# Optimization experiments

Hardware: AMD Instinct MI355X
Metric: run time of the kernel (lower is better)

## Reference

```python
import jax, jax.numpy as jnp
import numpy as np

N_NODES = 100000

def _sage_conv(h, src, dst, Wl, bl, Wr):
    # PyG SAGEConv (mean aggr): out = lin_l(mean_{j in N(i)} h_j) + lin_r(h_i)
    msg = h[src]                                            # [E, H] gather
    agg = jax.ops.segment_sum(msg, dst, num_segments=N_NODES)   # [N, H] scatter-add
    cnt = jax.ops.segment_sum(jnp.ones((src.shape[0],), h.dtype), dst, num_segments=N_NODES)
    mean = agg / jnp.maximum(cnt, 1.0)[:, None]
    return mean @ Wl + bl + h @ Wr

def setup_inputs() -> dict:
    key = jax.random.key(0)
    ks = jax.random.split(key, 12)
    IN, H, C, E = 256, 128, 40, 1600000
    s = 0.05
    return {
        "x": jax.random.normal(ks[0], (N_NODES, IN), jnp.float32),
        "edge_index": jax.random.randint(ks[1], (2, E), 0, N_NODES, jnp.int32),
        "W_pre": jax.random.normal(ks[2], (IN, H), jnp.float32) * s,
        "b_pre": jnp.zeros((H,), jnp.float32),
        "Wl0": jax.random.normal(ks[3], (H, H), jnp.float32) * s,
        "bl0": jnp.zeros((H,), jnp.float32),
        "Wr0": jax.random.normal(ks[4], (H, H), jnp.float32) * s,
        "Wl1": jax.random.normal(ks[5], (H, H), jnp.float32) * s,
        "bl1": jnp.zeros((H,), jnp.float32),
        "Wr1": jax.random.normal(ks[6], (H, H), jnp.float32) * s,
        "W_post": jax.random.normal(ks[7], (H, C), jnp.float32) * s,
        "b_post": jnp.zeros((C,), jnp.float32),
    }

def reference(x, edge_index, W_pre, b_pre, Wl0, bl0, Wr0, Wl1, bl1, Wr1, W_post, b_post):
    src, dst = edge_index[0], edge_index[1]
    h = x @ W_pre + b_pre                       # pre Linear
    # two SAGEConv layers + relu (dropout is identity in eval mode)
    h = jax.nn.relu(_sage_conv(h, src, dst, Wl0, bl0, Wr0))
    h = jax.nn.relu(_sage_conv(h, src, dst, Wl1, bl1, Wr1))
    logits = h @ W_post + b_post                # post Linear
    return jax.nn.log_softmax(logits, axis=1)
```

## Files before the change

### kernel.cpp

```cpp
#include <hip/hip_runtime.h>
#include <hip/hip_bf16.h>
#include <math.h>

#define N_NODES 100000
#define IN_F 256
#define HID 128
#define NCLS 40

#define NB 782
#define BN 128
#define NC 448
#define CSZ2 3584
#define CAP 4096

typedef __attribute__((ext_vector_type(8))) short short8;
typedef __attribute__((ext_vector_type(4))) float f32x4;

__device__ __forceinline__ short f2bf(float f){
  union { float f; unsigned u; } x; x.f = f;
  unsigned r = (x.u + 0x7fffu + ((x.u >> 16) & 1u)) >> 16;
  return (short)r;
}
__device__ __forceinline__ float bf2f(unsigned short u){
  union { unsigned u; float f; } x; x.u = ((unsigned)u) << 16;
  return x.f;
}

__global__ __launch_bounds__(256) void k_wprep(
    const float* __restrict__ Wpre, const float* __restrict__ Wl0,
    const float* __restrict__ Wr0,  const float* __restrict__ Wl1,
    const float* __restrict__ Wr1,  const float* __restrict__ Wpost,
    unsigned short* __restrict__ img)
{
  const int g = blockIdx.x*256 + threadIdx.x;
  if(g >= 13056) return;
  const int base = g*8;
  unsigned short v[8];
  if(base < 98304){
    const int which = base >> 15;
    const int idx = base & 32767;
    const int l = (idx >> 3) & 63, kb = (idx >> 9) & 7, ct = idx >> 12;
    const int col = ct*16 + (l & 15);
    const float* Wsrc; int kbase;
    if(which == 0){ Wsrc = Wpre; kbase = kb*32 + (l>>4)*8; }
    else{
      Wsrc = (which==1) ? ((kb<4) ? Wl0 : Wr0) : ((kb<4) ? Wl1 : Wr1);
      kbase = (kb&3)*32 + (l>>4)*8;
    }
    #pragma unroll
    for(int j = 0; j < 8; j++) v[j] = (unsigned short)f2bf(Wsrc[(size_t)(kbase+j)*HID + col]);
  } else {
    const int idx = base - 98304;
    const int l = (idx >> 3) & 63, kb = (idx >> 9) & 3, ct = idx >> 11;
    const int col = ct*16 + (l & 15);
    const int kbase = kb*32 + (l>>4)*8;
    #pragma unroll
    for(int j = 0; j < 8; j++)
      v[j] = (col < NCLS) ? (unsigned short)f2bf(Wpost[(size_t)(kbase+j)*NCLS + col]) : 0;
  }
  *reinterpret_cast<short8*>(img + base) = *reinterpret_cast<const short8*>(v);
}

__global__ __launch_bounds__(256) void k_hist(const int* __restrict__ dst, int E,
                                              int* __restrict__ cnt){
  __shared__ int hist[NB];
  const int c = blockIdx.x;
  for(int i = threadIdx.x; i < NB; i += 256) hist[i] = 0;
  __syncthreads();
  const int s0 = c*CSZ2, s1 = min(s0 + CSZ2, E);
  for(int i = s0 + threadIdx.x; i < s1; i += 256)
    atomicAdd(&hist[(unsigned)__builtin_nontemporal_load(dst + i) >> 7], 1);
  __syncthreads();
  for(int i = threadIdx.x; i < NB; i += 256) cnt[c*NB + i] = hist[i];
}

__global__ __launch_bounds__(256) void k_bscanA(const int* __restrict__ cnt,
                                                int* __restrict__ wbase,
                                                int* __restrict__ btot){
  __shared__ int s[256];
  const int b = blockIdx.x;
  const int t = threadIdx.x;
  int v0 = 0, v1 = 0;
  if(2*t < NC)     v0 = cnt[(2*t)*NB + b];
  if(2*t + 1 < NC) v1 = cnt[(2*t+1)*NB + b];
  s[t] = v0 + v1; __syncthreads();
  for(int d = 1; d < 256; d <<= 1){
    int add = (t >= d) ? s[t-d] : 0;
    __syncthreads();
    s[t] += add;
    __syncthreads();
  }
  const int ex = (t > 0) ? s[t-1] : 0;
  if(2*t < NC)     wbase[(2*t)*NB + b] = ex;
  if(2*t + 1 < NC) wbase[(2*t+1)*NB + b] = ex + v0;
  if(t == 255) btot[b] = s[255];
}

__global__ __launch_bounds__(1024) void k_bscanB(const int* __restrict__ btot,
                                                 int* __restrict__ bstart, int E){
  __shared__ int s[1024];
  const int t = threadIdx.x;
  int v = (t < NB) ? btot[t] : 0;
  s[t] = v; __syncthreads();
  for(int d = 1; d < 1024; d <<= 1){
    int add = (t >= d) ? s[t-d] : 0;
    __syncthreads();
    s[t] += add;
    __syncthreads();
  }
  if(t < NB) bstart[t] = s[t] - v;
  if(t == 0) bstart[NB] = E;
}

__global__ __launch_bounds__(256) void k_place(const int* __restrict__ src,
                                               const int* __restrict__ dst, int E,
                                               const int* __restrict__ wbase,
                                               const int* __restrict__ bstart,
                                               int* __restrict__ pk){
  const int g = blockIdx.x;
  const int c = (g & 7)*(NC/8) + (g >> 3);
  __shared__ int cur[NB];
  for(int i = threadIdx.x; i < NB; i += 256)
    cur[i] = wbase[c*NB + i] + bstart[i];
  __syncthreads();
  const int s0 = c*CSZ2, s1 = min(s0 + CSZ2, E);
  for(int i = s0 + threadIdx.x; i < s1; i += 256){
    const int d  = __builtin_nontemporal_load(dst + i);
    const int sv = __builtin_nontemporal_load(src + i);
    const int pos = atomicAdd(&cur[(unsigned)d >> 7], 1);
    pk[pos] = ((d & 127) << 17) | sv;
  }
}

__global__ __launch_bounds__(512) void k_agg_b(
    const unsigned short* __restrict__ h, const int* __restrict__ pk,
    const int* __restrict__ bstart, unsigned short* __restrict__ mean)
{
  __shared__ int stage[CAP];
  __shared__ int lists[CAP];
  __shared__ int hist[BN];
  __shared__ int nofs[BN];
  __shared__ int curs[BN];
  const int b = blockIdx.x;
  const int t = threadIdx.x;
  const int bs = bstart[b];
  const int be = bstart[b+1];
  const int ne = be - bs;
  const int wave = t >> 6, lane = t & 63;
  const unsigned* hp = (const unsigned*)h;

  if(ne <= CAP){
    for(int i = t; i < BN; i += 512) hist[i] = 0;
    __syncthreads();
    for(int i = t; i < ne; i += 512){
      const int e = __builtin_nontemporal_load(pk + bs + i);
      stage[i] = e;
      atomicAdd(&hist[e >> 17], 1);
    }
    __syncthreads();
    if(t < BN) nofs[t] = hist[t];
    __syncthreads();
    for(int d = 1; d < BN; d <<= 1){
      int add = 0;
      if(t < BN && t >= d) add = nofs[t-d];
      __syncthreads();
      if(t < BN) nofs[t] += add;
      __syncthreads();
    }
    if(t < BN) curs[t] = nofs[t] - hist[t];
    __syncthreads();
    for(int i = t; i < ne; i += 512){
      const int e = stage[i];
      const int pos = atomicAdd(&curs[e >> 17], 1);
      lists[pos] = e & 0x1ffff;
    }
    __syncthreads();
    for(int n = wave; n < BN; n += 8){
      const int node = b*BN + n;
      if(node >= N_NODES) break;
      const int deg = hist[n];
      const int nb_ = nofs[n] - deg;
      float a0 = 0.f, a1 = 0.f;
      int e = 0;
      for(; e + 8 <= deg; e += 8){
        unsigned v[8];
        #pragma unroll
        for(int u = 0; u < 8; u++){
          const int s = lists[nb_ + e + u];
          v[u] = hp[(size_t)s*64 + lane];
        }
        #pragma unroll
        for(int u = 0; u < 8; u++){
          a0 += bf2f((unsigned short)(v[u] & 0xffffu));
          a1 += bf2f((unsigned short)(v[u] >> 16));
        }
      }
      for(; e < deg; e++){
        const int s = lists[nb_ + e];
        const unsigned vv = hp[(size_t)s*64 + lane];
        a0 += bf2f((unsigned short)(vv & 0xffffu));
        a1 += bf2f((unsigned short)(vv >> 16));
      }
      const float inv = (deg > 0) ? (1.0f/(float)deg) : 0.f;
      a0 *= inv; a1 *= inv;
      const unsigned o = ((unsigned)(unsigned short)f2bf(a1) << 16) | (unsigned)(unsigned short)f2bf(a0);
      ((unsigned*)mean)[(size_t)node*64 + lane] = o;
    }
  } else {
    for(int n = wave; n < BN; n += 8){
      const int node = b*BN + n;
      if(node >= N_NODES) break;
      float a0 = 0.f, a1 = 0.f; int deg = 0;
      for(int i = 0; i < ne; i++){
        const int e = pk[bs + i];
        if((e >> 17) == n){
          const int s = e & 0x1ffff;
          const unsigned vv = hp[(size_t)s*64 + lane];
          a0 += bf2f((unsigned short)(vv & 0xffffu));
          a1 += bf2f((unsigned short)(vv >> 16));
          deg++;
        }
      }
      const float inv = (deg > 0) ? (1.0f/(float)deg) : 0.f;
      a0 *= inv; a1 *= inv;
      const unsigned o = ((unsigned)(unsigned short)f2bf(a1) << 16) | (unsigned)(unsigned short)f2bf(a0);
      ((unsigned*)mean)[(size_t)node*64 + lane] = o;
    }
  }
}

__global__ __launch_bounds__(256) void k_gemm_pre(
    const float* __restrict__ x, const unsigned short* __restrict__ wimg,
    const float* __restrict__ b, unsigned short* __restrict__ out)
{
  __shared__ short wlds[8*8*64*8];
  const int t = threadIdx.x;
  {
    short8* dstp = reinterpret_cast<short8*>(wlds);
    const short8* srcp = reinterpret_cast<const short8*>(wimg);
    #pragma unroll
    for(int i = 0; i < 16; i++) dstp[t + i*256] = srcp[t + i*256];
  }
  __syncthreads();
  const int wave = t >> 6, lane = t & 63;
  const int r_in = lane & 15, kg = lane >> 4;
  for(int tile = blockIdx.x*4 + wave; tile < N_NODES/16; tile += gridDim.x*4){
    const int row0 = tile*16;
    const float* xp = x + (size_t)(row0 + r_in)*IN_F + kg*8;
    float4 xa[8], xb[8];
    #pragma unroll
    for(int kb = 0; kb < 8; kb++){
      xa[kb] = *reinterpret_cast<const float4*>(xp + kb*32);
      xb[kb] = *reinterpret_cast<const float4*>(xp + kb*32 + 4);
    }
    f32x4 acc[8];
    #pragma unroll
    for(int ct = 0; ct < 8; ct++) acc[ct] = (f32x4){0.f,0.f,0.f,0.f};
    #pragma unroll
    for(int kb = 0; kb < 8; kb++){
      short8 a;
      a[0]=f2bf(xa[kb].x); a[1]=f2bf(xa[kb].y); a[2]=f2bf(xa[kb].z); a[3]=f2bf(xa[kb].w);
      a[4]=f2bf(xb[kb].x); a[5]=f2bf(xb[kb].y); a[6]=f2bf(xb[kb].z); a[7]=f2bf(xb[kb].w);
      #pragma unroll
      for(int ct = 0; ct < 8; ct++){
        short8 bb = *reinterpret_cast<const short8*>(&wlds[((ct*8+kb)*64+lane)*8]);
        acc[ct] = __builtin_amdgcn_mfma_f32_16x16x32_bf16(a, bb, acc[ct], 0, 0, 0);
      }
    }
    #pragma unroll
    for(int ct = 0; ct < 8; ct++){
      const int col = ct*16 + r_in;
      const float bias = b[col];
      #pragma unroll
      for(int i = 0; i < 4; i++){
        const int row = row0 + kg*4 + i;
        out[(size_t)row*HID + col] = (unsigned short)f2bf(acc[ct][i] + bias);
      }
    }
  }
}

__global__ __launch_bounds__(256) void k_gemm_sage(
    const unsigned short* __restrict__ mean, const unsigned short* __restrict__ h,
    const unsigned short* __restrict__ wimg, const float* __restrict__ bl,
    unsigned short* __restrict__ out)
{
  __shared__ short wlds[8*8*64*8];
  const int t = threadIdx.x;
  {
    short8* dstp = reinterpret_cast<short8*>(wlds);
    const short8* srcp = reinterpret_cast<const short8*>(wimg);
    #pragma unroll
    for(int i = 0; i < 16; i++) dstp[t + i*256] = srcp[t + i*256];
  }
  __syncthreads();
  const int wave = t >> 6, lane = t & 63;
  const int r_in = lane & 15, kg = lane >> 4;
  for(int tile = blockIdx.x*4 + wave; tile < N_NODES/16; tile += gridDim.x*4){
    const int row0 = tile*16;
    f32x4 acc[8];
    #pragma unroll
    for(int ct = 0; ct < 8; ct++) acc[ct] = (f32x4){0.f,0.f,0.f,0.f};
    #pragma unroll
    for(int kb = 0; kb < 8; kb++){
      const unsigned short* in = (kb < 4) ? mean : h;
      const int koff = (kb & 3)*32 + kg*8;
      short8 a = *reinterpret_cast<const short8*>(in + (size_t)(row0 + r_in)*HID + koff);
      #pragma unroll
      for(int ct = 0; ct < 8; ct++){
        short8 bb = *reinterpret_cast<const short8*>(&wlds[((ct*8+kb)*64+lane)*8]);
        acc[ct] = __builtin_amdgcn_mfma_f32_16x16x32_bf16(a, bb, acc[ct], 0, 0, 0);
      }
    }
    #pragma unroll
    for(int ct = 0; ct < 8; ct++){
      const int col = ct*16 + r_in;
      const float bias = bl[col];
      #pragma unroll
      for(int i = 0; i < 4; i++){
        const int row = row0 + kg*4 + i;
        float v = fmaxf(acc[ct][i] + bias, 0.f);
        out[(size_t)row*HID + col] = (unsigned short)f2bf(v);
      }
    }
  }
}

__global__ __launch_bounds__(256) void k_post(
    const unsigned short* __restrict__ h, const unsigned short* __restrict__ wimg,
    const float* __restrict__ b, float* __restrict__ out)
{
  __shared__ short wlds[3*4*64*8];
  __shared__ float bias_s[48];
  const int t = threadIdx.x;
  {
    short8* dstp = reinterpret_cast<short8*>(wlds);
    const short8* srcp = reinterpret_cast<const short8*>(wimg);
    for(int i = t; i < 768; i += 256) dstp[i] = srcp[i];
  }
  if(t < 48) bias_s[t] = (t < NCLS) ? b[t] : -1e30f;
  __syncthreads();
  const int wave = t >> 6, lane = t & 63;
  const int r_in = lane & 15, kg = lane >> 4;
  for(int tile = blockIdx.x*4 + wave; tile < N_NODES/16; tile += gridDim.x*4){
    const int row0 = tile*16;
    f32x4 acc[3];
    #pragma unroll
    for(int ct = 0; ct < 3; ct++) acc[ct] = (f32x4){0.f,0.f,0.f,0.f};
    #pragma unroll
    for(int kb = 0; kb < 4; kb++){
      short8 a = *reinterpret_cast<const short8*>(h + (size_t)(row0 + r_in)*HID + kb*32 + kg*8);
      #pragma unroll
      for(int ct = 0; ct < 3; ct++){
        short8 bb = *reinterpret_cast<const short8*>(&wlds[((ct*4+kb)*64+lane)*8]);
        acc[ct] = __builtin_amdgcn_mfma_f32_16x16x32_bf16(a, bb, acc[ct], 0, 0, 0);
      }
    }
    #pragma unroll
    for(int i = 0; i < 4; i++){
      float v0 = acc[0][i] + bias_s[r_in];
      float v1 = acc[1][i] + bias_s[16 + r_in];
      float v2 = acc[2][i] + bias_s[32 + r_in];
      float m = fmaxf(fmaxf(v0, v1), v2);
      #pragma unroll
      for(int o = 8; o > 0; o >>= 1) m = fmaxf(m, __shfl_xor(m, o));
      float s = expf(v0 - m) + expf(v1 - m) + expf(v2 - m);
      #pragma unroll
      for(int o = 8; o > 0; o >>= 1) s += __shfl_xor(s, o);
      const float ls = m + logf(s);
      const int row = row0 + kg*4 + i;
      float* op = out + (size_t)row*NCLS;
      op[r_in] = v0 - ls;
      op[16 + r_in] = v1 - ls;
      if(r_in < 8) op[32 + r_in] = v2 - ls;
    }
  }
}

extern "C" void kernel_launch(void* const* d_in, const int* in_sizes, int n_in,
                              void* d_out, int out_size, void* d_ws, size_t ws_size,
                              hipStream_t stream)
{
  const float* x      = (const float*)d_in[0];
  const int*   ei     = (const int*)  d_in[1];
  const float* W_pre  = (const float*)d_in[2];
  const float* b_pre  = (const float*)d_in[3];
  const float* Wl0    = (const float*)d_in[4];
  const float* bl0    = (const float*)d_in[5];
  const float* Wr0    = (const float*)d_in[6];
  const float* Wl1    = (const float*)d_in[7];
  const float* bl1    = (const float*)d_in[8];
  const float* Wr1    = (const float*)d_in[9];
  const float* W_post = (const float*)d_in[10];
  const float* b_post = (const float*)d_in[11];
  float* out = (float*)d_out;

  const int E = in_sizes[1] / 2;
  const int* src = ei;
  const int* dst = ei + E;

  char* ws = (char*)d_ws;
  size_t off = 0;
  auto alloc = [&](size_t bytes)->void*{
    void* p = ws + off;
    off += (bytes + 255) & ~(size_t)255;
    return p;
  };
  unsigned short* hA = (unsigned short*)alloc((size_t)N_NODES*HID*2);
  unsigned short* hB = (unsigned short*)alloc((size_t)N_NODES*HID*2);
  unsigned short* hM = (unsigned short*)alloc((size_t)N_NODES*HID*2);
  int* pk     = (int*)alloc((size_t)E*4);
  int* cnt    = (int*)alloc((size_t)NC*NB*4);
  int* wbase  = (int*)alloc((size_t)NC*NB*4);
  int* btot   = (int*)alloc((size_t)NB*4);
  int* bstart = (int*)alloc((size_t)(NB+1)*4);
  unsigned short* wimg = (unsigned short*)alloc(104448*2);

  k_wprep<<<51, 256, 0, stream>>>(W_pre, Wl0, Wr0, Wl1, Wr1, W_post, wimg);

  k_hist<<<NC, 256, 0, stream>>>(dst, E, cnt);
  k_bscanA<<<NB, 256, 0, stream>>>(cnt, wbase, btot);
  k_bscanB<<<1, 1024, 0, stream>>>(btot, bstart, E);
  k_place<<<NC, 256, 0, stream>>>(src, dst, E, wbase, bstart, pk);

  k_gemm_pre<<<512, 256, 0, stream>>>(x, wimg, b_pre, hA);

  k_agg_b<<<NB, 512, 0, stream>>>(hA, pk, bstart, hM);
  k_gemm_sage<<<1563, 256, 0, stream>>>(hM, hA, wimg + 32768, bl0, hB);

  k_agg_b<<<NB, 512, 0, stream>>>(hB, pk, bstart, hM);
  k_gemm_sage<<<1563, 256, 0, stream>>>(hM, hB, wimg + 65536, bl1, hA);

  k_post<<<1563, 256, 0, stream>>>(hA, wimg + 98304, b_post, out);
}
```

Baseline: 280.0 us.

## Build global CSR once and aggregate with wave-per-node gather kernel

Moves the per-bucket counting sort out of the aggregation kernel into a separate one-time k_sortb pass that writes a global CSR (nodeoff, esrc2). Both layers then use k_agg3, a grid-stride wave-per-node kernel that loads 64 neighbor indices coalesced and broadcasts them with readlane. This removes the duplicated in-kernel sort and the 32KB of LDS per block, which should raise occupancy. It costs an extra E-sized buffer and one more kernel launch.

```diff
diff --git a/kernel.cpp b/kernel.cpp
--- a/kernel.cpp
+++ b/kernel.cpp
@@ -11,7 +11,6 @@
 #define BN 128
 #define NC 448
 #define CSZ2 3584
-#define CAP 4096
 
 typedef __attribute__((ext_vector_type(8))) short short8;
 typedef __attribute__((ext_vector_type(4))) float f32x4;
@@ -132,61 +131,67 @@
   }
 }
 
-__global__ __launch_bounds__(512) void k_agg_b(
-    const unsigned short* __restrict__ h, const int* __restrict__ pk,
-    const int* __restrict__ bstart, unsigned short* __restrict__ mean)
-{
-  __shared__ int stage[CAP];
-  __shared__ int lists[CAP];
+__global__ __launch_bounds__(512) void k_sortb(const int* __restrict__ pk,
+                                               const int* __restrict__ bstart,
+                                               int* __restrict__ esrc2,
+                                               int* __restrict__ nodeoff, int E){
   __shared__ int hist[BN];
   __shared__ int nofs[BN];
   __shared__ int curs[BN];
   const int b = blockIdx.x;
   const int t = threadIdx.x;
   const int bs = bstart[b];
-  const int be = bstart[b+1];
-  const int ne = be - bs;
-  const int wave = t >> 6, lane = t & 63;
+  const int ne = bstart[b+1] - bs;
+  for(int i = t; i < BN; i += 512) hist[i] = 0;
+  __syncthreads();
+  for(int i = t; i < ne; i += 512)
+    atomicAdd(&hist[(unsigned)pk[bs + i] >> 17], 1);
+  __syncthreads();
+  if(t < BN) nofs[t] = hist[t];
+  __syncthreads();
+  for(int d = 1; d < BN; d <<= 1){
+    int add = 0;
+    if(t < BN && t >= d) add = nofs[t-d];
+    __syncthreads();
+    if(t < BN) nofs[t] += add;
+    __syncthreads();
+  }
+  if(t < BN){
+    curs[t] = nofs[t] - hist[t];
+    const int node = b*BN + t;
+    if(node < N_NODES) nodeoff[node] = bs + nofs[t] - hist[t];
+    if(node == N_NODES - 1 || (b == NB-1 && t == BN-1)) nodeoff[N_NODES] = E;
+  }
+  __syncthreads();
+  for(int i = t; i < ne; i += 512){
+    const int e = pk[bs + i];
+    const int pos = atomicAdd(&curs[(unsigned)e >> 17], 1);
+    esrc2[bs + pos] = e & 0x1ffff;
+  }
+}
+
+__global__ __launch_bounds__(256) void k_agg3(
+    const unsigned short* __restrict__ h, const int* __restrict__ nodeoff,
+    const int* __restrict__ esrc2, unsigned short* __restrict__ mean)
+{
+  const int lane = threadIdx.x & 63;
+  const int wid = blockIdx.x*4 + (threadIdx.x >> 6);
+  const int wstride = gridDim.x*4;
   const unsigned* hp = (const unsigned*)h;
-
-  if(ne <= CAP){
-    for(int i = t; i < BN; i += 512) hist[i] = 0;
-    __syncthreads();
-    for(int i = t; i < ne; i += 512){
-      const int e = __builtin_nontemporal_load(pk + bs + i);
-      stage[i] = e;
-      atomicAdd(&hist[e >> 17], 1);
-    }
-    __syncthreads();
-    if(t < BN) nofs[t] = hist[t];
-    __syncthreads();
-    for(int d = 1; d < BN; d <<= 1){
-      int add = 0;
-      if(t < BN && t >= d) add = nofs[t-d];
-      __syncthreads();
-      if(t < BN) nofs[t] += add;
-      __syncthreads();
-    }
-    if(t < BN) curs[t] = nofs[t] - hist[t];
-    __syncthreads();
-    for(int i = t; i < ne; i += 512){
-      const int e = stage[i];
-      const int pos = atomicAdd(&curs[e >> 17], 1);
-      lists[pos] = e & 0x1ffff;
-    }
-    __syncthreads();
-    for(int n = wave; n < BN; n += 8){
-      const int node = b*BN + n;
-      if(node >= N_NODES) break;
-      const int deg = hist[n];
-      const int nb_ = nofs[n] - deg;
-      float a0 = 0.f, a1 = 0.f;
+  for(int node = wid; node < N_NODES; node += wstride){
+    const int beg = nodeoff[node];
+    const int deg = nodeoff[node+1] - beg;
+    float a0 = 0.f, a1 = 0.f;
+    for(int base = 0; base < deg; base += 64){
+      const int rem = deg - base;
+      const int cnt = rem < 64 ? rem : 64;
+      const int myi = (lane < cnt) ? esrc2[beg + base + lane] : 0;
       int e = 0;
-      for(; e + 8 <= deg; e += 8){
+      for(; e + 8 <= cnt; e += 8){
         unsigned v[8];
         #pragma unroll
         for(int u = 0; u < 8; u++){
-          const int s = lists[nb_ + e + u];
+          const int s = __builtin_amdgcn_readlane(myi, e + u);
           v[u] = hp[(size_t)s*64 + lane];
         }
         #pragma unroll
@@ -195,37 +200,17 @@
           a1 += bf2f((unsigned short)(v[u] >> 16));
         }
       }
-      for(; e < deg; e++){
-        const int s = lists[nb_ + e];
+      for(; e < cnt; e++){
+        const int s = __builtin_amdgcn_readlane(myi, e);
         const unsigned vv = hp[(size_t)s*64 + lane];
         a0 += bf2f((unsigned short)(vv & 0xffffu));
         a1 += bf2f((unsigned short)(vv >> 16));
       }
-      const float inv = (deg > 0) ? (1.0f/(float)deg) : 0.f;
-      a0 *= inv; a1 *= inv;
-      const unsigned o = ((unsigned)(unsigned short)f2bf(a1) << 16) | (unsigned)(unsigned short)f2bf(a0);
-      ((unsigned*)mean)[(size_t)node*64 + lane] = o;
-    }
-  } else {
-    for(int n = wave; n < BN; n += 8){
-      const int node = b*BN + n;
-      if(node >= N_NODES) break;
-      float a0 = 0.f, a1 = 0.f; int deg = 0;
-      for(int i = 0; i < ne; i++){
-        const int e = pk[bs + i];
-        if((e >> 17) == n){
-          const int s = e & 0x1ffff;
-          const unsigned vv = hp[(size_t)s*64 + lane];
-          a0 += bf2f((unsigned short)(vv & 0xffffu));
-          a1 += bf2f((unsigned short)(vv >> 16));
-          deg++;
-        }
-      }
-      const float inv = (deg > 0) ? (1.0f/(float)deg) : 0.f;
-      a0 *= inv; a1 *= inv;
-      const unsigned o = ((unsigned)(unsigned short)f2bf(a1) << 16) | (unsigned)(unsigned short)f2bf(a0);
-      ((unsigned*)mean)[(size_t)node*64 + lane] = o;
-    }
+    }
+    const float inv = (deg > 0) ? (1.0f/(float)deg) : 0.f;
+    a0 *= inv; a1 *= inv;
+    const unsigned o = ((unsigned)(unsigned short)f2bf(a1) << 16) | (unsigned)(unsigned short)f2bf(a0);
+    ((unsigned*)mean)[(size_t)node*64 + lane] = o;
   }
 }
 
@@ -409,11 +394,13 @@
   unsigned short* hA = (unsigned short*)alloc((size_t)N_NODES*HID*2);
   unsigned short* hB = (unsigned short*)alloc((size_t)N_NODES*HID*2);
   unsigned short* hM = (unsigned short*)alloc((size_t)N_NODES*HID*2);
-  int* pk     = (int*)alloc((size_t)E*4);
-  int* cnt    = (int*)alloc((size_t)NC*NB*4);
-  int* wbase  = (int*)alloc((size_t)NC*NB*4);
-  int* btot   = (int*)alloc((size_t)NB*4);
-  int* bstart = (int*)alloc((size_t)(NB+1)*4);
+  int* pk      = (int*)alloc((size_t)E*4);
+  int* esrc2   = (int*)alloc((size_t)E*4);
+  int* cnt     = (int*)alloc((size_t)NC*NB*4);
+  int* wbase   = (int*)alloc((size_t)NC*NB*4);
+  int* btot    = (int*)alloc((size_t)NB*4);
+  int* bstart  = (int*)alloc((size_t)(NB+1)*4);
+  int* nodeoff = (int*)alloc((size_t)(N_NODES+1)*4);
   unsigned short* wimg = (unsigned short*)alloc(104448*2);
 
   k_wprep<<<51, 256, 0, stream>>>(W_pre, Wl0, Wr0, Wl1, Wr1, W_post, wimg);
@@ -422,13 +409,14 @@
   k_bscanA<<<NB, 256, 0, stream>>>(cnt, wbase, btot);
   k_bscanB<<<1, 1024, 0, stream>>>(btot, bstart, E);
   k_place<<<NC, 256, 0, stream>>>(src, dst, E, wbase, bstart, pk);
+  k_sortb<<<NB, 512, 0, stream>>>(pk, bstart, esrc2, nodeoff, E);
 
   k_gemm_pre<<<512, 256, 0, stream>>>(x, wimg, b_pre, hA);
 
-  k_agg_b<<<NB, 512, 0, stream>>>(hA, pk, bstart, hM);
+  k_agg3<<<4096, 256, 0, stream>>>(hA, nodeoff, esrc2, hM);
   k_gemm_sage<<<1563, 256, 0, stream>>>(hM, hA, wimg + 32768, bl0, hB);
 
-  k_agg_b<<<NB, 512, 0, stream>>>(hB, pk, bstart, hM);
+  k_agg3<<<4096, 256, 0, stream>>>(hB, nodeoff, esrc2, hM);
   k_gemm_sage<<<1563, 256, 0, stream>>>(hM, hB, wimg + 65536, bl1, hA);
 
   k_post<<<1563, 256, 0, stream>>>(hA, wimg + 98304, b_post, out);
```

New measurement: 285.9 us. 1.02x slower.
